# Kernel optimization log

Hardware: AMD Instinct MI355X
Metric: run time of the kernel (lower is better)

The kernel has to match this reference:

```python
import jax, jax.numpy as jnp
import numpy as np

B, T, D, H = 8, 1024, 512, 8
D4 = 4 * D
SIGMA = 16.0
EPS = 1e-5


def layer_norm(x, w, b):
    m = jnp.mean(x, axis=-1, keepdims=True)
    v = jnp.mean((x - m) ** 2, axis=-1, keepdims=True)
    return (x - m) * jax.lax.rsqrt(v + EPS) * w + b


def setup_inputs() -> dict:
    key = jax.random.key(0)
    ks = jax.random.split(key, 12)
    return {
        "x": jax.random.normal(ks[0], (B, T, D), jnp.float32),
        "posv": jax.random.randint(ks[1], (B, T), 0, 64, jnp.int32),
        "posh": jax.random.randint(ks[2], (B, T), 0, 64, jnp.int32),
        "norm1_w": jnp.ones((D,), jnp.float32),
        "norm1_b": jnp.zeros((D,), jnp.float32),
        "in_w": jax.random.normal(ks[3], (3 * D, D), jnp.float32) * (D ** -0.5),
        "in_b": jnp.zeros((3 * D,), jnp.float32),
        "out_w": jax.random.normal(ks[4], (D, D), jnp.float32) * (D ** -0.5),
        "out_b": jnp.zeros((D,), jnp.float32),
        "norm2_w": jnp.ones((D,), jnp.float32),
        "norm2_b": jnp.zeros((D,), jnp.float32),
        "w1": jax.random.normal(ks[5], (D4, D), jnp.float32) * (D ** -0.5),
        "b1": jnp.zeros((D4,), jnp.float32),
        "w2": jax.random.normal(ks[6], (D, D4), jnp.float32) * (D4 ** -0.5),
        "b2": jnp.zeros((D,), jnp.float32),
        "gate": jnp.array(0.0, jnp.float32),
    }


def reference(x, posv, posh, norm1_w, norm1_b, in_w, in_b, out_w, out_b,
              norm2_w, norm2_b, w1, b1, w2, b2, gate):
    hd = D // H
    residual = x
    xn = layer_norm(x, norm1_w, norm1_b)

    # --- standard multi-head self-attention (dropout=eval identity) ---
    qkv = xn @ in_w.T + in_b                       # [B,T,3D]
    q, k, v = jnp.split(qkv, 3, axis=-1)
    q = q.reshape(B, T, H, hd).transpose(0, 2, 1, 3)  # [B,H,T,hd]
    k = k.reshape(B, T, H, hd).transpose(0, 2, 1, 3)
    v = v.reshape(B, T, H, hd).transpose(0, 2, 1, 3)
    scores = jnp.einsum("bhqd,bhkd->bhqk", q, k) * (hd ** -0.5)
    attn = jax.nn.softmax(scores, axis=-1)
    ctx = jnp.einsum("bhqk,bhkd->bhqd", attn, v)   # [B,H,T,hd]
    ctx = ctx.transpose(0, 2, 1, 3).reshape(B, T, D)
    std_out = ctx @ out_w.T + out_b

    # --- Gaussian kernel position attention ---
    pos = jnp.stack([posv, posh], axis=-1).astype(jnp.float32)  # [B,T,2]
    dist_sq = jnp.sum((pos[:, :, None, :] - pos[:, None, :, :]) ** 2, axis=-1)  # [B,T,T]
    kw = jnp.exp(-dist_sq / (2.0 * SIGMA ** 2))
    kw = kw / jnp.sum(kw, axis=-1, keepdims=True)
    kernel_out = kw @ xn                            # [B,T,D]

    g = jax.nn.sigmoid(gate)
    x1 = residual + g * std_out + (1.0 - g) * kernel_out

    # --- MLP block ---
    xn2 = layer_norm(x1, norm2_w, norm2_b)
    h = jax.nn.gelu(xn2 @ w1.T + b1, approximate=False)
    return x1 + h @ w2.T + b2
```

## Files before the change

kernel.cpp:

```cpp
#include <hip/hip_runtime.h>
#include <hip/hip_bf16.h>
#include <math.h>

typedef unsigned short ushort_t;
typedef short short8 __attribute__((ext_vector_type(8)));
typedef float f32x4 __attribute__((ext_vector_type(4)));

__device__ __forceinline__ float b2f(ushort_t u) {
  union { unsigned u; float f; } v; v.u = ((unsigned)u) << 16; return v.f;
}
__device__ __forceinline__ ushort_t f2b(float f) {
  union { float f; unsigned u; } v; v.f = f;
  unsigned r = (v.u + 0x7FFFu + ((v.u >> 16) & 1u)) >> 16;
  return (ushort_t)r;
}
__device__ __forceinline__ float gelu_fast(float v) {
  float u = 0.7978845608f * (v + 0.044715f * v * v * v);
  float a = fabsf(u);
  float t = exp2f(a * -2.8853900817779268f);
  float th = (1.f - t) / (1.f + t);
  th = copysignf(th, u);
  return 0.5f * v * (1.f + th);
}

union U16x8 { uint4 v; ushort_t s[8]; };

typedef const __attribute__((address_space(1))) unsigned int glb_u32;
typedef __attribute__((address_space(3))) unsigned int lds_u32;
__device__ __forceinline__ void gl_lds16(const ushort_t* g, ushort_t* l) {
  __builtin_amdgcn_global_load_lds((glb_u32*)g, (lds_u32*)l, 16, 0, 0);
}

__global__ __launch_bounds__(256) void cvt4_kernel(const float* __restrict__ s0,
                                                   const float* __restrict__ s1,
                                                   const float* __restrict__ s2,
                                                   const float* __restrict__ s3,
                                                   ushort_t* __restrict__ d0,
                                                   ushort_t* __restrict__ d1,
                                                   ushort_t* __restrict__ d2,
                                                   ushort_t* __restrict__ d3) {
  long i = (long)blockIdx.x * 256 + threadIdx.x;
  const float* s; ushort_t* d; long off;
  if (i < 196608)       { s = s0; d = d0; off = i; }
  else if (i < 262144)  { s = s1; d = d1; off = i - 196608; }
  else if (i < 524288)  { s = s2; d = d2; off = i - 262144; }
  else                  { s = s3; d = d3; off = i - 524288; }
  float4 f = *(const float4*)(s + off * 4);
  union { uint2 v; ushort_t s[4]; } o;
  o.s[0] = f2b(f.x); o.s[1] = f2b(f.y); o.s[2] = f2b(f.z); o.s[3] = f2b(f.w);
  *(uint2*)(d + off * 4) = o.v;
}

__global__ __launch_bounds__(256) void ln_kernel(const float* __restrict__ x,
                                                 const float* __restrict__ w,
                                                 const float* __restrict__ b,
                                                 ushort_t* __restrict__ out) {
  int tid = threadIdx.x, wave = tid >> 6, lane = tid & 63;
  long token = (long)blockIdx.x * 4 + wave;
  const float* xr = x + token * 512 + lane * 8;
  float4 a0 = *(const float4*)xr;
  float4 a1 = *(const float4*)(xr + 4);
  float xf[8] = {a0.x, a0.y, a0.z, a0.w, a1.x, a1.y, a1.z, a1.w};
  float s = 0.f, sq = 0.f;
#pragma unroll
  for (int i = 0; i < 8; i++) { s += xf[i]; sq += xf[i] * xf[i]; }
#pragma unroll
  for (int off = 1; off < 64; off <<= 1) { s += __shfl_xor(s, off); sq += __shfl_xor(sq, off); }
  float m = s * (1.f / 512.f);
  float var = sq * (1.f / 512.f) - m * m;
  float rs = rsqrtf(var + 1e-5f);
  float4 w0 = *(const float4*)(w + lane * 8);
  float4 w1v = *(const float4*)(w + lane * 8 + 4);
  float4 b0 = *(const float4*)(b + lane * 8);
  float4 b1v = *(const float4*)(b + lane * 8 + 4);
  float wf[8] = {w0.x, w0.y, w0.z, w0.w, w1v.x, w1v.y, w1v.z, w1v.w};
  float bf[8] = {b0.x, b0.y, b0.z, b0.w, b1v.x, b1v.y, b1v.z, b1v.w};
  U16x8 o;
#pragma unroll
  for (int i = 0; i < 8; i++) o.s[i] = f2b((xf[i] - m) * rs * wf[i] + bf[i]);
  *(uint4*)(out + token * 512 + lane * 8) = o.v;
}

__global__ __launch_bounds__(256) void ln_b_kernel(const ushort_t* __restrict__ x,
                                                   const float* __restrict__ w,
                                                   const float* __restrict__ b,
                                                   ushort_t* __restrict__ out) {
  int tid = threadIdx.x, wave = tid >> 6, lane = tid & 63;
  long token = (long)blockIdx.x * 4 + wave;
  U16x8 ux; ux.v = *(const uint4*)(x + token * 512 + lane * 8);
  float xf[8], s = 0.f, sq = 0.f;
#pragma unroll
  for (int i = 0; i < 8; i++) { xf[i] = b2f(ux.s[i]); s += xf[i]; sq += xf[i] * xf[i]; }
#pragma unroll
  for (int off = 1; off < 64; off <<= 1) { s += __shfl_xor(s, off); sq += __shfl_xor(sq, off); }
  float m = s * (1.f / 512.f);
  float var = sq * (1.f / 512.f) - m * m;
  float rs = rsqrtf(var + 1e-5f);
  float4 w0 = *(const float4*)(w + lane * 8);
  float4 w1v = *(const float4*)(w + lane * 8 + 4);
  float4 b0 = *(const float4*)(b + lane * 8);
  float4 b1v = *(const float4*)(b + lane * 8 + 4);
  float wf[8] = {w0.x, w0.y, w0.z, w0.w, w1v.x, w1v.y, w1v.z, w1v.w};
  float bf[8] = {b0.x, b0.y, b0.z, b0.w, b1v.x, b1v.y, b1v.z, b1v.w};
  U16x8 o;
#pragma unroll
  for (int i = 0; i < 8; i++) o.s[i] = f2b((xf[i] - m) * rs * wf[i] + bf[i]);
  *(uint4*)(out + token * 512 + lane * 8) = o.v;
}

__global__ __launch_bounds__(256) void kw_kernel(const int* __restrict__ posv,
                                                 const int* __restrict__ posh,
                                                 ushort_t* __restrict__ kw) {
  int b = blockIdx.x >> 10, i = blockIdx.x & 1023;
  int tid = threadIdx.x;
  const int* pv = posv + b * 1024;
  const int* ph = posh + b * 1024;
  int pvi = pv[i], phi = ph[i];
  int j0 = tid * 4;
  int4 vj = *(const int4*)(pv + j0);
  int4 hj = *(const int4*)(ph + j0);
  int vv[4] = {vj.x, vj.y, vj.z, vj.w};
  int hh[4] = {hj.x, hj.y, hj.z, hj.w};
  float e[4]; float loc = 0.f;
#pragma unroll
  for (int u = 0; u < 4; u++) {
    int dv = pvi - vv[u], dh = phi - hh[u];
    e[u] = expf((float)(dv * dv + dh * dh) * (-1.f / 512.f));
    loc += e[u];
  }
#pragma unroll
  for (int off = 1; off < 64; off <<= 1) loc += __shfl_xor(loc, off);
  __shared__ float wsum[4];
  __shared__ float tot;
  if ((tid & 63) == 0) wsum[tid >> 6] = loc;
  __syncthreads();
  if (tid == 0) tot = wsum[0] + wsum[1] + wsum[2] + wsum[3];
  __syncthreads();
  float inv = 1.f / tot;
  union { uint2 v; ushort_t s[4]; } o;
#pragma unroll
  for (int u = 0; u < 4; u++) o.s[u] = f2b(e[u] * inv);
  *(uint2*)&kw[((long)(b * 1024 + i)) * 1024 + j0] = o.v;
}

__global__ __launch_bounds__(256) void tr_kernel(const ushort_t* __restrict__ in,
                                                 ushort_t* __restrict__ out,
                                                 int R, int C) {
  __shared__ ushort_t tile[64 * 64];
  int z = blockIdx.z, r0 = blockIdx.y * 64, c0 = blockIdx.x * 64;
  const ushort_t* src = in + (long)z * R * C;
  ushort_t* dst = out + (long)z * R * C;
  int tid = threadIdx.x;
  int tr = tid >> 2;
  const ushort_t* s = src + (long)(r0 + tr) * C + c0;
  int g = (tr + (tr >> 4)) & 7;
#pragma unroll
  for (int u = 0; u < 2; u++) {
    int c = (tid & 3) + u * 4;
    *(uint4*)&tile[tr * 64 + (c ^ g) * 8] = *(const uint4*)(s + c * 8);
  }
  __syncthreads();
  int oc = tid >> 2, ob = (tid & 3) * 16;
  U16x8 o0, o1;
#pragma unroll
  for (int j = 0; j < 16; j++) {
    int r = ob + j;
    int gg = (r + (r >> 4)) & 7;
    ushort_t val = tile[r * 64 + (((oc >> 3) ^ gg)) * 8 + (oc & 7)];
    if (j < 8) o0.s[j] = val; else o1.s[j - 8] = val;
  }
  ushort_t* d = dst + (long)(c0 + oc) * R + r0 + ob;
  *(uint4*)d = o0.v;
  *(uint4*)(d + 8) = o1.v;
}

struct GemmP {
  const ushort_t* A; const ushort_t* Bm;
  long sA, sB, sC;
  int lda, ldb, ldc, K;
  const float* biasf;
  const float* residf;
  const ushort_t* auxb;
  const float* auxf;
  float* outf;
  ushort_t* outb;
  ushort_t* qp; ushort_t* kp; ushort_t* vp;
  const float* gate;
};

template <int BM, int BN, int EPI>
__global__ __launch_bounds__(256) void gemm_k(GemmP p) {
  constexpr int TI = BM / 32, TJ = BN / 32;
  constexpr int RA = BM / 64, RB = BN / 64;
  __shared__ ushort_t As[2][BM * 32];
  __shared__ ushort_t Bs[2][BN * 32];
  int tid = threadIdx.x, wv = tid >> 6, lane = tid & 63;
  int quad = lane >> 4, l15 = lane & 15;
  int bl = blockIdx.x + gridDim.x * blockIdx.y;
  int m0 = (bl % gridDim.y) * BM;
  int n0 = (bl / gridDim.y) * BN;
  int z = blockIdx.z;
  const ushort_t* A = p.A + (long)z * p.sA;
  const ushort_t* Bm = p.Bm + (long)z * p.sB;
  int wm = (wv & 1) * (BM / 2), wn = (wv >> 1) * (BN / 2);
  f32x4 acc[TI][TJ];
#pragma unroll
  for (int i = 0; i < TI; i++)
#pragma unroll
    for (int j = 0; j < TJ; j++)
#pragma unroll
      for (int r = 0; r < 4; r++) acc[i][j][r] = 0.f;

  int srow = tid >> 2;
  int sc = ((tid & 3) ^ ((tid >> 3) & 3)) * 8;
  const ushort_t* ga = A + (long)(m0 + srow) * p.lda + sc;
  const ushort_t* gb = Bm + (long)(n0 + srow) * p.ldb + sc;
  long a64 = (long)64 * p.lda, b64 = (long)64 * p.ldb;
  int aswz = (quad ^ ((l15 >> 1) & 3)) * 8;
  int nsteps = p.K >> 5;

#pragma unroll
  for (int rr = 0; rr < RA; rr++)
    gl_lds16(ga + rr * a64, As[0] + rr * 2048 + wv * 512);
#pragma unroll
  for (int rr = 0; rr < RB; rr++)
    gl_lds16(gb + rr * b64, Bs[0] + rr * 2048 + wv * 512);
  __syncthreads();

  for (int ks = 0; ks < nsteps; ks++) {
    int cur = ks & 1;
    if (ks + 1 < nsteps) {
      const ushort_t* a0 = ga + (ks + 1) * 32;
      const ushort_t* b0 = gb + (ks + 1) * 32;
#pragma unroll
      for (int rr = 0; rr < RA; rr++)
        gl_lds16(a0 + rr * a64, As[cur ^ 1] + rr * 2048 + wv * 512);
#pragma unroll
      for (int rr = 0; rr < RB; rr++)
        gl_lds16(b0 + rr * b64, Bs[cur ^ 1] + rr * 2048 + wv * 512);
    }
    short8 av[TI], bv[TJ];
#pragma unroll
    for (int ti = 0; ti < TI; ti++)
      av[ti] = *(const short8*)&As[cur][(wm + ti * 16 + l15) * 32 + aswz];
#pragma unroll
    for (int tj = 0; tj < TJ; tj++)
      bv[tj] = *(const short8*)&Bs[cur][(wn + tj * 16 + l15) * 32 + aswz];
#pragma unroll
    for (int ti = 0; ti < TI; ti++)
#pragma unroll
      for (int tj = 0; tj < TJ; tj++)
        acc[ti][tj] = __builtin_amdgcn_mfma_f32_16x16x32_bf16(av[ti], bv[tj], acc[ti][tj], 0, 0, 0);
    __syncthreads();
  }

  float g = 0.f;
  if constexpr (EPI == 2) g = 1.f / (1.f + expf(-p.gate[0]));
#pragma unroll
  for (int ti = 0; ti < TI; ti++) {
#pragma unroll
    for (int tj = 0; tj < TJ; tj++) {
#pragma unroll
      for (int r = 0; r < 4; r++) {
        int gm = m0 + wm + ti * 16 + quad * 4 + r;
        int n = n0 + wn + tj * 16 + l15;
        float v = acc[ti][tj][r];
        if constexpr (EPI == 0) {
          v += p.biasf[n];
          int bb = gm >> 10, tt = gm & 1023;
          if (n < 512) {
            int h = n >> 6, d = n & 63;
            p.qp[((long)(bb * 8 + h) * 1024 + tt) * 64 + d] = f2b(v * 0.18033688011112042f);
          } else if (n < 1024) {
            int n2 = n - 512, h = n2 >> 6, d = n2 & 63;
            p.kp[((long)(bb * 8 + h) * 1024 + tt) * 64 + d] = f2b(v);
          } else {
            int n2 = n - 1024, h = n2 >> 6, d = n2 & 63;
            p.vp[((long)(bb * 8 + h) * 1024 + tt) * 64 + d] = f2b(v);
          }
        } else if constexpr (EPI == 1) {
          p.outb[(long)z * p.sC + (long)gm * p.ldc + n] = f2b(v);
        } else if constexpr (EPI == 2) {
          v += p.biasf[n];
          long idx = (long)gm * 512 + n;
          p.outb[idx] = f2b(p.residf[idx] + g * v + (1.f - g) * b2f(p.auxb[idx]));
        } else if constexpr (EPI == 3) {
          v += p.biasf[n];
          p.outb[(long)gm * p.ldc + n] = f2b(gelu_fast(v));
        } else {
          v += p.biasf[n];
          long idx = (long)gm * 512 + n;
          p.outf[idx] = v + b2f(p.auxb[idx]);
        }
      }
    }
  }
}

template <int EPI>
__global__ __launch_bounds__(512, 2) void gemm256_k(GemmP p) {
  __shared__ __align__(16) ushort_t As[2][256 * 64];
  __shared__ __align__(16) ushort_t Bs[2][256 * 64];
  int tid = threadIdx.x, wv = tid >> 6, lane = tid & 63;
  int quad = lane >> 4, l15 = lane & 15;
  int m0 = blockIdx.x * 256, n0 = blockIdx.y * 256;
  int wr = wv >> 2, wc = wv & 3;

  int srow = tid >> 3;
  int scol = ((tid & 7) ^ (srow & 7)) * 8;
  const ushort_t* ga = p.A + (long)(m0 + srow) * p.lda + scol;
  const ushort_t* gb = p.Bm + (long)(n0 + srow) * p.ldb + scol;
  long a64 = (long)64 * p.lda, b64 = (long)64 * p.ldb;
  int NT = p.K >> 6;

  f32x4 acc[8][4];
#pragma unroll
  for (int i = 0; i < 8; i++)
#pragma unroll
    for (int j = 0; j < 4; j++)
#pragma unroll
      for (int r = 0; r < 4; r++) acc[i][j][r] = 0.f;

  gl_lds16(gb + 0 * b64, Bs[0] + 0 * 4096 + wv * 512);
  gl_lds16(gb + 1 * b64, Bs[0] + 1 * 4096 + wv * 512);
  gl_lds16(gb + 2 * b64, Bs[0] + 2 * 4096 + wv * 512);
  gl_lds16(gb + 3 * b64, Bs[0] + 3 * 4096 + wv * 512);
  gl_lds16(ga + 0 * a64, As[0] + 0 * 4096 + wv * 512);
  gl_lds16(ga + 2 * a64, As[0] + 2 * 4096 + wv * 512);
  gl_lds16(ga + 1 * a64, As[0] + 1 * 4096 + wv * 512);
  gl_lds16(ga + 3 * a64, As[0] + 3 * 4096 + wv * 512);
  asm volatile("s_waitcnt vmcnt(2)" ::: "memory");
  __builtin_amdgcn_s_barrier();

  int c0 = (quad ^ (l15 & 7)) * 8;
  int c1 = ((quad + 4) ^ (l15 & 7)) * 8;

  for (int t = 0; t < NT; t++) {
    int bt = t & 1, nx = bt ^ 1;
    bool pre = (t + 1 < NT);
    const ushort_t* Ab = &As[bt][(wr * 128 + l15) * 64];
    const ushort_t* Bb = &Bs[bt][(wc * 64 + l15) * 64];
    const ushort_t* gak = ga + (t + 1) * 64;
    const ushort_t* gbk = gb + (t + 1) * 64;
    short8 a[8], bn0[4], bn1[4];

#pragma unroll
    for (int mf = 0; mf < 4; mf++) {
      a[2 * mf]     = *(const short8*)(Ab + mf * 1024 + c0);
      a[2 * mf + 1] = *(const short8*)(Ab + mf * 1024 + c1);
    }
#pragma unroll
    for (int nf = 0; nf < 2; nf++) {
      bn0[2 * nf]     = *(const short8*)(Bb + nf * 1024 + c0);
      bn0[2 * nf + 1] = *(const short8*)(Bb + nf * 1024 + c1);
    }
    if (pre) {
      gl_lds16(gbk + 0 * b64, Bs[nx] + 0 * 4096 + wv * 512);
      gl_lds16(gbk + 1 * b64, Bs[nx] + 1 * 4096 + wv * 512);
    }
    __builtin_amdgcn_s_barrier();
    __builtin_amdgcn_s_setprio(1);
#pragma unroll
    for (int mf = 0; mf < 4; mf++)
#pragma unroll
      for (int nf = 0; nf < 2; nf++) {
        acc[mf][nf] = __builtin_amdgcn_mfma_f32_16x16x32_bf16(a[2 * mf], bn0[2 * nf], acc[mf][nf], 0, 0, 0);
        acc[mf][nf] = __builtin_amdgcn_mfma_f32_16x16x32_bf16(a[2 * mf + 1], bn0[2 * nf + 1], acc[mf][nf], 0, 0, 0);
      }
    __builtin_amdgcn_s_setprio(0);
    __builtin_amdgcn_s_barrier();

#pragma unroll
    for (int nf = 0; nf < 2; nf++) {
      bn1[2 * nf]     = *(const short8*)(Bb + (2 + nf) * 1024 + c0);
      bn1[2 * nf + 1] = *(const short8*)(Bb + (2 + nf) * 1024 + c1);
    }
    if (pre) {
      gl_lds16(gbk + 2 * b64, Bs[nx] + 2 * 4096 + wv * 512);
      gl_lds16(gbk + 3 * b64, Bs[nx] + 3 * 4096 + wv * 512);
    }
    __builtin_amdgcn_s_barrier();
    __builtin_amdgcn_s_setprio(1);
#pragma unroll
    for (int mf = 0; mf < 4; mf++)
#pragma unroll
      for (int nf = 0; nf < 2; nf++) {
        acc[mf][2 + nf] = __builtin_amdgcn_mfma_f32_16x16x32_bf16(a[2 * mf], bn1[2 * nf], acc[mf][2 + nf], 0, 0, 0);
        acc[mf][2 + nf] = __builtin_amdgcn_mfma_f32_16x16x32_bf16(a[2 * mf + 1], bn1[2 * nf + 1], acc[mf][2 + nf], 0, 0, 0);
      }
    __builtin_amdgcn_s_setprio(0);
    if (pre) asm volatile("s_waitcnt vmcnt(4)" ::: "memory");
    else     asm volatile("s_waitcnt vmcnt(0)" ::: "memory");
    __builtin_amdgcn_s_barrier();

#pragma unroll
    for (int mf = 0; mf < 4; mf++) {
      a[2 * mf]     = *(const short8*)(Ab + (4 + mf) * 1024 + c0);
      a[2 * mf + 1] = *(const short8*)(Ab + (4 + mf) * 1024 + c1);
    }
    if (pre) {
      gl_lds16(gak + 0 * a64, As[nx] + 0 * 4096 + wv * 512);
      gl_lds16(gak + 2 * a64, As[nx] + 2 * 4096 + wv * 512);
    }
    __builtin_amdgcn_s_barrier();
    __builtin_amdgcn_s_setprio(1);
#pragma unroll
    for (int mf = 0; mf < 4; mf++)
#pragma unroll
      for (int nf = 0; nf < 2; nf++) {
        acc[4 + mf][2 + nf] = __builtin_amdgcn_mfma_f32_16x16x32_bf16(a[2 * mf], bn1[2 * nf], acc[4 + mf][2 + nf], 0, 0, 0);
        acc[4 + mf][2 + nf] = __builtin_amdgcn_mfma_f32_16x16x32_bf16(a[2 * mf + 1], bn1[2 * nf + 1], acc[4 + mf][2 + nf], 0, 0, 0);
      }
    __builtin_amdgcn_s_setprio(0);
    __builtin_amdgcn_s_barrier();

    if (pre) {
      gl_lds16(gak + 1 * a64, As[nx] + 1 * 4096 + wv * 512);
      gl_lds16(gak + 3 * a64, As[nx] + 3 * 4096 + wv * 512);
    }
    __builtin_amdgcn_s_barrier();
    __builtin_amdgcn_s_setprio(1);
#pragma unroll
    for (int mf = 0; mf < 4; mf++)
#pragma unroll
      for (int nf = 0; nf < 2; nf++) {
        acc[4 + mf][nf] = __builtin_amdgcn_mfma_f32_16x16x32_bf16(a[2 * mf], bn0[2 * nf], acc[4 + mf][nf], 0, 0, 0);
        acc[4 + mf][nf] = __builtin_amdgcn_mfma_f32_16x16x32_bf16(a[2 * mf + 1], bn0[2 * nf + 1], acc[4 + mf][nf], 0, 0, 0);
      }
    __builtin_amdgcn_s_setprio(0);
    if (pre) asm volatile("s_waitcnt vmcnt(2)" ::: "memory");
    __builtin_amdgcn_s_barrier();
  }

#pragma unroll
  for (int mf = 0; mf < 8; mf++) {
#pragma unroll
    for (int nf = 0; nf < 4; nf++) {
#pragma unroll
      for (int r = 0; r < 4; r++) {
        int gm = m0 + wr * 128 + mf * 16 + quad * 4 + r;
        int n = n0 + wc * 64 + nf * 16 + l15;
        float v = acc[mf][nf][r];
        if constexpr (EPI == 0) {
          v += p.biasf[n];
          int bb = gm >> 10, tt = gm & 1023;
          if (n < 512) {
            int h = n >> 6, d = n & 63;
            p.qp[((long)(bb * 8 + h) * 1024 + tt) * 64 + d] = f2b(v * 0.18033688011112042f);
          } else if (n < 1024) {
            int n2 = n - 512, h = n2 >> 6, d = n2 & 63;
            p.kp[((long)(bb * 8 + h) * 1024 + tt) * 64 + d] = f2b(v);
          } else {
            int n2 = n - 1024, h = n2 >> 6, d = n2 & 63;
            p.vp[((long)(bb * 8 + h) * 1024 + tt) * 64 + d] = f2b(v);
          }
        } else {
          v += p.biasf[n];
          p.outb[(long)gm * p.ldc + n] = f2b(gelu_fast(v));
        }
      }
    }
  }
}

__global__ __launch_bounds__(256) void flash_k(const ushort_t* __restrict__ q,
                                               const ushort_t* __restrict__ k,
                                               const ushort_t* __restrict__ vT,
                                               ushort_t* __restrict__ ctx) {
  int bl = blockIdx.x + gridDim.x * blockIdx.y;
  int bh = bl % 64;
  int q0 = (bl / 64) * 128;
  int tid = threadIdx.x, wv = tid >> 6, lane = tid & 63;
  int quad = lane >> 4, l15 = lane & 15;
  __shared__ ushort_t Ks[2][64 * 64], Vt[2][64 * 64];
  __shared__ ushort_t Pt[128 * 64];
  int wm = wv * 32;

  short8 qf[2][2];
#pragma unroll
  for (int tq = 0; tq < 2; tq++)
#pragma unroll
    for (int kk = 0; kk < 2; kk++)
      qf[tq][kk] = *(const short8*)&q[((long)bh * 1024 + q0 + wm + tq * 16 + l15) * 64 + kk * 32 + quad * 8];

  int srow = tid >> 3;
  int sc = ((tid & 7) ^ ((tid >> 3) & 7)) * 8;
#pragma unroll
  for (int e = 0; e < 2; e++) {
    gl_lds16(&k[((long)bh * 1024 + e * 32 + srow) * 64 + sc], Ks[0] + e * 2048 + wv * 512);
    gl_lds16(&vT[((long)bh * 64 + e * 32 + srow) * 1024 + sc], Vt[0] + e * 2048 + wv * 512);
  }
  __syncthreads();

  f32x4 O[2][4];
#pragma unroll
  for (int tq = 0; tq < 2; tq++)
#pragma unroll
    for (int td = 0; td < 4; td++)
#pragma unroll
      for (int r = 0; r < 4; r++) O[tq][td][r] = 0.f;
  float ls[2] = {0.f, 0.f};

  int pswz = (l15 & 7) << 1;
  for (int kt = 0; kt < 16; kt++) {
    int cur = kt & 1;
    if (kt + 1 < 16) {
#pragma unroll
      for (int e = 0; e < 2; e++) {
        gl_lds16(&k[((long)bh * 1024 + (kt + 1) * 64 + e * 32 + srow) * 64 + sc], Ks[cur ^ 1] + e * 2048 + wv * 512);
        gl_lds16(&vT[((long)bh * 64 + e * 32 + srow) * 1024 + (kt + 1) * 64 + sc], Vt[cur ^ 1] + e * 2048 + wv * 512);
      }
    }
#pragma unroll
    for (int tq = 0; tq < 2; tq++) {
      f32x4 S[4];
#pragma unroll
      for (int tk = 0; tk < 4; tk++) {
#pragma unroll
        for (int r = 0; r < 4; r++) S[tk][r] = 0.f;
#pragma unroll
        for (int kk = 0; kk < 2; kk++) {
          short8 kf = *(const short8*)&Ks[cur][(tk * 16 + l15) * 64 + ((kk * 4 + quad) ^ (l15 & 7)) * 8];
          S[tk] = __builtin_amdgcn_mfma_f32_16x16x32_bf16(kf, qf[tq][kk], S[tk], 0, 0, 0);
        }
      }
#pragma unroll
      for (int tk = 0; tk < 4; tk++) {
        float p0 = exp2f(S[tk][0]);
        float p1 = exp2f(S[tk][1]);
        float p2 = exp2f(S[tk][2]);
        float p3 = exp2f(S[tk][3]);
        ls[tq] += (p0 + p1) + (p2 + p3);
        unsigned lo = __builtin_amdgcn_perm(__float_as_uint(p1), __float_as_uint(p0), 0x07060302u);
        unsigned hi = __builtin_amdgcn_perm(__float_as_uint(p3), __float_as_uint(p2), 0x07060302u);
        int gnum = (tk * 4 + quad) ^ pswz;
        uint2 pr; pr.x = lo; pr.y = hi;
        *(uint2*)&Pt[(wm + tq * 16 + l15) * 64 + gnum * 4] = pr;
      }
    }
#pragma unroll
    for (int tq = 0; tq < 2; tq++) {
#pragma unroll
      for (int kk = 0; kk < 2; kk++) {
        short8 pf = *(const short8*)&Pt[(wm + tq * 16 + l15) * 64 + (((kk * 8 + quad * 2) ^ pswz)) * 4];
#pragma unroll
        for (int td = 0; td < 4; td++) {
          short8 vf = *(const short8*)&Vt[cur][(td * 16 + l15) * 64 + ((kk * 4 + quad) ^ (l15 & 7)) * 8];
          O[tq][td] = __builtin_amdgcn_mfma_f32_16x16x32_bf16(pf, vf, O[tq][td], 0, 0, 0);
        }
      }
    }
    __syncthreads();
  }
#pragma unroll
  for (int tq = 0; tq < 2; tq++) {
    ls[tq] += __shfl_xor(ls[tq], 16);
    ls[tq] += __shfl_xor(ls[tq], 32);
  }
  int bb = bh >> 3, h = bh & 7;
#pragma unroll
  for (int tq = 0; tq < 2; tq++) {
#pragma unroll
    for (int r = 0; r < 4; r++) {
      int qrow = quad * 4 + r;
      float inv = 1.f / __shfl(ls[tq], (lane & 48) | qrow);
      long row = (long)bb * 1024 + q0 + wm + tq * 16 + qrow;
#pragma unroll
      for (int td = 0; td < 4; td++)
        ctx[row * 512 + h * 64 + td * 16 + l15] = f2b(O[tq][td][r] * inv);
    }
  }
}

extern "C" void kernel_launch(void* const* d_in, const int* in_sizes, int n_in,
                              void* d_out, int out_size, void* d_ws, size_t ws_size,
                              hipStream_t stream) {
  const float* x    = (const float*)d_in[0];
  const int* posv   = (const int*)d_in[1];
  const int* posh   = (const int*)d_in[2];
  const float* n1w  = (const float*)d_in[3];
  const float* n1b  = (const float*)d_in[4];
  const float* in_w = (const float*)d_in[5];
  const float* in_b = (const float*)d_in[6];
  const float* outw = (const float*)d_in[7];
  const float* outb = (const float*)d_in[8];
  const float* n2w  = (const float*)d_in[9];
  const float* n2b  = (const float*)d_in[10];
  const float* w1   = (const float*)d_in[11];
  const float* b1   = (const float*)d_in[12];
  const float* w2   = (const float*)d_in[13];
  const float* b2   = (const float*)d_in[14];
  const float* gate = (const float*)d_in[15];
  float* out = (float*)d_out;

  char* ws = (char*)d_ws;
  const size_t MB = 1024 * 1024;
  ushort_t* q    = (ushort_t*)(ws + 0 * MB);
  ushort_t* kk   = (ushort_t*)(ws + 8 * MB);
  ushort_t* vtmp = (ushort_t*)(ws + 16 * MB);
  ushort_t* vT   = (ushort_t*)(ws + 24 * MB);
  ushort_t* kw   = (ushort_t*)(ws + 32 * MB);
  ushort_t* xn   = (ushort_t*)(ws + 48 * MB);
  ushort_t* xnT  = (ushort_t*)(ws + 56 * MB);
  ushort_t* ctx  = (ushort_t*)(ws + 64 * MB);
  ushort_t* ko   = (ushort_t*)(ws + 72 * MB);
  ushort_t* x1b  = (ushort_t*)(ws + 80 * MB);
  ushort_t* xn2  = (ushort_t*)(ws + 16 * MB);
  ushort_t* inwb = (ushort_t*)(ws + 96 * MB);
  ushort_t* owb  = (ushort_t*)(ws + 98 * MB);
  ushort_t* w1b  = (ushort_t*)(ws + 99 * MB);
  ushort_t* w2b  = (ushort_t*)(ws + 101 * MB);
  ushort_t* h    = (ushort_t*)(ws + 24 * MB);

  cvt4_kernel<<<3072, 256, 0, stream>>>(in_w, outw, w1, w2, inwb, owb, w1b, w2b);
  ln_kernel<<<2048, 256, 0, stream>>>(x, n1w, n1b, xn);
  kw_kernel<<<8192, 256, 0, stream>>>(posv, posh, kw);
  {
    GemmP p = {};
    p.A = xn; p.Bm = inwb; p.lda = 512; p.ldb = 512; p.K = 512;
    p.biasf = in_b; p.qp = q; p.kp = kk; p.vp = vtmp;
    gemm256_k<0><<<dim3(32, 6), 512, 0, stream>>>(p);
  }
  tr_kernel<<<dim3(1, 16, 64), 256, 0, stream>>>(vtmp, vT, 1024, 64);
  flash_k<<<dim3(8, 64, 1), 256, 0, stream>>>(q, kk, vT, ctx);
  tr_kernel<<<dim3(8, 16, 8), 256, 0, stream>>>(xn, xnT, 1024, 512);
  {
    GemmP p = {};
    p.A = kw; p.Bm = xnT; p.lda = 1024; p.ldb = 1024; p.ldc = 512; p.K = 1024;
    p.sA = 1024L * 1024; p.sB = 512L * 1024; p.sC = 1024L * 512;
    p.outb = ko;
    gemm_k<64, 128, 1><<<dim3(4, 16, 8), 256, 0, stream>>>(p);
  }
  {
    GemmP p = {};
    p.A = ctx; p.Bm = owb; p.lda = 512; p.ldb = 512; p.K = 512;
    p.biasf = outb; p.residf = x; p.auxb = ko; p.outb = x1b; p.gate = gate;
    gemm_k<64, 64, 2><<<dim3(8, 128, 1), 256, 0, stream>>>(p);
  }
  ln_b_kernel<<<2048, 256, 0, stream>>>(x1b, n2w, n2b, xn2);
  {
    GemmP p = {};
    p.A = xn2; p.Bm = w1b; p.lda = 512; p.ldb = 512; p.ldc = 2048; p.K = 512;
    p.biasf = b1; p.outb = h;
    gemm256_k<3><<<dim3(32, 8), 512, 0, stream>>>(p);
  }
  {
    GemmP p = {};
    p.A = h; p.Bm = w2b; p.lda = 2048; p.ldb = 2048; p.K = 2048;
    p.biasf = b2; p.auxb = x1b; p.outf = out;
    gemm_k<64, 128, 4><<<dim3(4, 128, 1), 256, 0, stream>>>(p);
  }
}
```

Before: 298.7 us.

## Deepen gemm_k LDS pipeline to four stages and remap blocks per XCD

The generic GEMM kernel now uses four LDS buffers and prefetches two K-steps at a time, so it synchronises once per pair of 32-wide K-steps instead of once per step. Both GEMM kernels also remap the linear block index so consecutive tiles land on the same XCD (groups of 8), which is meant to improve L2 reuse across the chiplets. The cost is double the shared memory in gemm_k, which may lower occupancy. The remap assumes the block count is divisible by 8.

```diff
diff --git a/kernel.cpp b/kernel.cpp
--- a/kernel.cpp
+++ b/kernel.cpp
@@ -192,11 +192,13 @@
 __global__ __launch_bounds__(256) void gemm_k(GemmP p) {
   constexpr int TI = BM / 32, TJ = BN / 32;
   constexpr int RA = BM / 64, RB = BN / 64;
-  __shared__ ushort_t As[2][BM * 32];
-  __shared__ ushort_t Bs[2][BN * 32];
+  __shared__ ushort_t As[4][BM * 32];
+  __shared__ ushort_t Bs[4][BN * 32];
   int tid = threadIdx.x, wv = tid >> 6, lane = tid & 63;
   int quad = lane >> 4, l15 = lane & 15;
   int bl = blockIdx.x + gridDim.x * blockIdx.y;
+  int nwg = gridDim.x * gridDim.y;
+  bl = (bl & 7) * (nwg >> 3) + (bl >> 3);
   int m0 = (bl % gridDim.y) * BM;
   int n0 = (bl / gridDim.y) * BN;
   int z = blockIdx.z;
@@ -220,37 +222,47 @@
   int nsteps = p.K >> 5;
 
 #pragma unroll
-  for (int rr = 0; rr < RA; rr++)
-    gl_lds16(ga + rr * a64, As[0] + rr * 2048 + wv * 512);
-#pragma unroll
-  for (int rr = 0; rr < RB; rr++)
-    gl_lds16(gb + rr * b64, Bs[0] + rr * 2048 + wv * 512);
+  for (int s = 0; s < 2; s++) {
+#pragma unroll
+    for (int rr = 0; rr < RA; rr++)
+      gl_lds16(ga + s * 32 + rr * a64, As[s] + rr * 2048 + wv * 512);
+#pragma unroll
+    for (int rr = 0; rr < RB; rr++)
+      gl_lds16(gb + s * 32 + rr * b64, Bs[s] + rr * 2048 + wv * 512);
+  }
   __syncthreads();
 
-  for (int ks = 0; ks < nsteps; ks++) {
-    int cur = ks & 1;
-    if (ks + 1 < nsteps) {
-      const ushort_t* a0 = ga + (ks + 1) * 32;
-      const ushort_t* b0 = gb + (ks + 1) * 32;
-#pragma unroll
-      for (int rr = 0; rr < RA; rr++)
-        gl_lds16(a0 + rr * a64, As[cur ^ 1] + rr * 2048 + wv * 512);
-#pragma unroll
-      for (int rr = 0; rr < RB; rr++)
-        gl_lds16(b0 + rr * b64, Bs[cur ^ 1] + rr * 2048 + wv * 512);
-    }
-    short8 av[TI], bv[TJ];
-#pragma unroll
-    for (int ti = 0; ti < TI; ti++)
-      av[ti] = *(const short8*)&As[cur][(wm + ti * 16 + l15) * 32 + aswz];
-#pragma unroll
-    for (int tj = 0; tj < TJ; tj++)
-      bv[tj] = *(const short8*)&Bs[cur][(wn + tj * 16 + l15) * 32 + aswz];
-#pragma unroll
-    for (int ti = 0; ti < TI; ti++)
+  for (int ks = 0; ks < nsteps; ks += 2) {
+    if (ks + 2 < nsteps) {
+#pragma unroll
+      for (int s = 0; s < 2; s++) {
+        int st = ks + 2 + s, bf = st & 3;
+        const ushort_t* a0 = ga + st * 32;
+        const ushort_t* b0 = gb + st * 32;
+#pragma unroll
+        for (int rr = 0; rr < RA; rr++)
+          gl_lds16(a0 + rr * a64, As[bf] + rr * 2048 + wv * 512);
+#pragma unroll
+        for (int rr = 0; rr < RB; rr++)
+          gl_lds16(b0 + rr * b64, Bs[bf] + rr * 2048 + wv * 512);
+      }
+    }
+#pragma unroll
+    for (int hs = 0; hs < 2; hs++) {
+      int cur = (ks + hs) & 3;
+      short8 av[TI], bv[TJ];
+#pragma unroll
+      for (int ti = 0; ti < TI; ti++)
+        av[ti] = *(const short8*)&As[cur][(wm + ti * 16 + l15) * 32 + aswz];
 #pragma unroll
       for (int tj = 0; tj < TJ; tj++)
-        acc[ti][tj] = __builtin_amdgcn_mfma_f32_16x16x32_bf16(av[ti], bv[tj], acc[ti][tj], 0, 0, 0);
+        bv[tj] = *(const short8*)&Bs[cur][(wn + tj * 16 + l15) * 32 + aswz];
+#pragma unroll
+      for (int ti = 0; ti < TI; ti++)
+#pragma unroll
+        for (int tj = 0; tj < TJ; tj++)
+          acc[ti][tj] = __builtin_amdgcn_mfma_f32_16x16x32_bf16(av[ti], bv[tj], acc[ti][tj], 0, 0, 0);
+    }
     __syncthreads();
   }
 
@@ -303,7 +315,11 @@
   __shared__ __align__(16) ushort_t Bs[2][256 * 64];
   int tid = threadIdx.x, wv = tid >> 6, lane = tid & 63;
   int quad = lane >> 4, l15 = lane & 15;
-  int m0 = blockIdx.x * 256, n0 = blockIdx.y * 256;
+  int bl = blockIdx.x + gridDim.x * blockIdx.y;
+  int nwg = gridDim.x * gridDim.y;
+  bl = (bl & 7) * (nwg >> 3) + (bl >> 3);
+  int m0 = (bl % gridDim.x) * 256;
+  int n0 = (bl / gridDim.x) * 256;
   int wr = wv >> 2, wc = wv & 3;
 
   int srow = tid >> 3;
```

After: 394.6 us. +32.1%, slower.
